# Performance work log

Measured on AMD Instinct MI355X. Metric: run time of the kernel, lower is better.

## Reference

```python
import jax, jax.numpy as jnp
import numpy as np

B, T, EMB, HS = 4, 4096, 1024, 64
BASE = 10000.0


def rope_angles(T, hs, base=BASE):
    # theta_i = base^(-2i/hs), freqs[t, i] = t * theta_i  -> (T, hs//2)
    inv = 1.0 / (base ** (2.0 * jnp.arange(hs // 2, dtype=jnp.float32) / hs))
    return jnp.arange(T, dtype=jnp.float32)[:, None] * inv[None, :]


def apply_rope(x, cos, sin):
    # x: (B, T, D); pairs are interleaved (even, odd) like torch.view_as_complex
    xr = x.reshape(*x.shape[:-1], -1, 2)
    xe, xo = xr[..., 0], xr[..., 1]
    re = xe * cos - xo * sin
    im = xe * sin + xo * cos
    return jnp.stack([re, im], axis=-1).reshape(x.shape)


def setup_inputs() -> dict:
    key = jax.random.key(0)
    kx, kq, kk, kv = jax.random.split(key, 4)
    s = 1.0 / np.sqrt(EMB)
    return {
        "x": jax.random.normal(kx, (B, T, EMB), jnp.float32),
        "Wq": jax.random.normal(kq, (HS, EMB), jnp.float32) * s,
        "Wk": jax.random.normal(kk, (HS, EMB), jnp.float32) * s,
        "Wv": jax.random.normal(kv, (HS, EMB), jnp.float32) * s,
    }


def reference(x, Wq, Wk, Wv):
    Tlen = x.shape[1]
    ang = rope_angles(Tlen, HS)          # (T, HS//2)
    cos, sin = jnp.cos(ang), jnp.sin(ang)
    q = x @ Wq.T                          # (B, T, HS)
    k = x @ Wk.T
    v = x @ Wv.T
    q = apply_rope(q, cos, sin)
    k = apply_rope(k, cos, sin)
    scores = jnp.einsum("bqd,bkd->bqk", q, k) * (HS ** -0.5)
    causal = jnp.tril(jnp.ones((Tlen, Tlen), dtype=bool))
    scores = jnp.where(causal[None], scores, -jnp.inf)
    w = jax.nn.softmax(scores, axis=-1)   # dropout in eval mode: identity
    return jnp.einsum("bqk,bkd->bqd", w, v)
```

## Files before the change

### kernel.cpp

```cpp
#include <hip/hip_runtime.h>

typedef __bf16 bf16x8 __attribute__((ext_vector_type(8)));
typedef __bf16 bf16x4 __attribute__((ext_vector_type(4)));
typedef float f32x4 __attribute__((ext_vector_type(4)));
typedef float f32x16 __attribute__((ext_vector_type(16)));
typedef unsigned int u32;

#define T_LEN 4096

__device__ __forceinline__ f32x4 mfma16(bf16x8 a, bf16x8 b, f32x4 c) {
    return __builtin_amdgcn_mfma_f32_16x16x32_bf16(a, b, c, 0, 0, 0);
}
__device__ __forceinline__ f32x16 mfma32(bf16x8 a, bf16x8 b, f32x16 c) {
    return __builtin_amdgcn_mfma_f32_32x32x16_bf16(a, b, c, 0, 0, 0);
}
__device__ __forceinline__ u32 packbf(float lo, float hi) {
    union { __bf16 e[2]; u32 w; } u;
    u.e[0] = (__bf16)lo; u.e[1] = (__bf16)hi;
    return u.w;
}
__device__ __forceinline__ f32x16 zero16() {
    f32x16 z;
    #pragma unroll
    for (int i = 0; i < 16; i++) z[i] = 0.f;
    return z;
}

__global__ __launch_bounds__(256) void convert_w_kernel(
    const float* __restrict__ Wq, const float* __restrict__ Wk,
    const float* __restrict__ Wv, __bf16* __restrict__ wf)
{
    int e = (blockIdx.x * 256 + threadIdx.x) * 4;
    int frag = e >> 9;
    int wi = e & 511;
    int l = wi >> 3, j = wi & 7;
    int ft = frag / 12, fn = frag - ft * 12;
    int n = fn * 16 + (l & 15);
    int k = (ft >> 1) * 64 + (ft & 1) * 32 + ((l >> 4) & 3) * 8 + j;
    const float* src = (n < 64 ? Wq : (n < 128 ? Wk : Wv))
                     + (size_t)(n & 63) * 1024 + k;
    float4 f = *(const float4*)src;
    bf16x4 h = {(__bf16)f.x, (__bf16)f.y, (__bf16)f.z, (__bf16)f.w};
    *(bf16x4*)(wf + e) = h;
}

__global__ __launch_bounds__(512, 2) void proj_kernel(
    const float* __restrict__ x, const __bf16* __restrict__ wf,
    __bf16* __restrict__ qfb, __bf16* __restrict__ kfb, __bf16* __restrict__ vfb)
{
    __shared__ __bf16 smem[6144];
    __bf16 (*xs)[32][72] = (__bf16(*)[32][72])smem;
    __bf16* stage = smem;

    const int tid  = threadIdx.x;
    const int wave = tid >> 6, lane = tid & 63;
    const int l15 = lane & 15, l4 = lane >> 4;
    const int wm = wave >> 2, wn = wave & 3;
    const size_t m0 = (size_t)blockIdx.x * 32;
    const int xrow = tid >> 4, xc4 = (tid & 15) * 4;

    f32x4 acc[3];
    #pragma unroll
    for (int bn = 0; bn < 3; bn++) acc[bn] = (f32x4){0.f, 0.f, 0.f, 0.f};

    const float* xsrc = x + (m0 + xrow) * 1024 + xc4;
    const __bf16* wfw = wf + (size_t)(wn * 3) * 512 + lane * 8;

    float4 rxA, rxB;
    bf16x8 wA[3][2], wB[3][2];

    {
        float4 r0 = *(const float4*)(xsrc);
        bf16x4 hx = {(__bf16)r0.x, (__bf16)r0.y, (__bf16)r0.z, (__bf16)r0.w};
        *(bf16x4*)&xs[0][xrow][xc4] = hx;
        rxA = *(const float4*)(xsrc + 64);
        #pragma unroll
        for (int nf = 0; nf < 3; nf++)
            #pragma unroll
            for (int c = 0; c < 2; c++)
                wA[nf][c] = *(const bf16x8*)(wfw + (size_t)(c * 12 + nf) * 512);
    }
    __syncthreads();

    for (int t = 0; t < 16; t++) {
        const int cur = t & 1;
        if (t < 14)
            rxB = *(const float4*)(xsrc + (t + 2) * 64);
        if (t < 15) {
            const __bf16* wnx = wfw + (size_t)((t + 1) * 2) * 12 * 512;
            #pragma unroll
            for (int nf = 0; nf < 3; nf++)
                #pragma unroll
                for (int c = 0; c < 2; c++)
                    wB[nf][c] = *(const bf16x8*)(wnx + (size_t)(c * 12 + nf) * 512);
        }
        bf16x8 af[2];
        #pragma unroll
        for (int c = 0; c < 2; c++)
            af[c] = *(const bf16x8*)&xs[cur][wm * 16 + l15][c * 32 + l4 * 8];
        #pragma unroll
        for (int nf = 0; nf < 3; nf++)
            #pragma unroll
            for (int c = 0; c < 2; c++)
                acc[nf] = mfma16(af[c], wA[nf][c], acc[nf]);
        if (t < 15) {
            bf16x4 hx = {(__bf16)rxA.x, (__bf16)rxA.y, (__bf16)rxA.z, (__bf16)rxA.w};
            *(bf16x4*)&xs[cur ^ 1][xrow][xc4] = hx;
        }
        #pragma unroll
        for (int nf = 0; nf < 3; nf++)
            #pragma unroll
            for (int c = 0; c < 2; c++)
                wA[nf][c] = wB[nf][c];
        rxA = rxB;
        __syncthreads();
    }

    const int tq0 = (int)(m0 & 4095);
    #pragma unroll
    for (int nf = 0; nf < 3; nf++) {
        int n = wn * 48 + nf * 16 + l15;
        #pragma unroll
        for (int r = 0; r < 4; r++) {
            int row = wm * 16 + l4 * 4 + r;
            float val = acc[nf][r];
            float partner = __shfl_xor(val, 1);
            if (n < 128) {
                int i = (n & 63) >> 1;
                float ang = (float)(tq0 + row)
                          * __builtin_exp2f((float)i * (-13.287712379549449f / 32.f));
                float sn, cs;
                __sincosf(ang, &sn, &cs);
                float res = (n & 1) ? (partner * sn + val * cs)
                                    : (val * cs - partner * sn);
                if (n < 64) {
                    res *= 0.180336884f;
                    int d = n;
                    stage[(d >> 4) * 512 + (row + ((d >> 3) & 1) * 32) * 8 + (d & 7)]
                        = (__bf16)res;
                } else {
                    int d = n - 64;
                    int l31i = ((row >> 2) & 1) * 16 + ((row >> 4) & 1) * 8
                             + ((row >> 3) & 1) * 4 + (row & 3);
                    stage[2048 + (d >> 4) * 512
                          + (l31i + ((d >> 3) & 1) * 32) * 8 + (d & 7)] = (__bf16)res;
                }
            } else {
                int d = n - 128;
                int cc = ((d >> 5) << 1) | ((row & 31) >> 4);
                stage[4096 + cc * 512
                      + ((d & 31) + ((row >> 3) & 1) * 32) * 8 + (row & 7)]
                    = (__bf16)val;
            }
        }
    }
    __syncthreads();
    {
        const size_t bbase = (size_t)(m0 >> 12) * 262144;
        const size_t tbase = (size_t)((m0 & 4095) >> 5) * 2048;
        bf16x4 q4 = *(const bf16x4*)&stage[tid * 4];
        bf16x4 k4 = *(const bf16x4*)&stage[2048 + tid * 4];
        bf16x4 v4 = *(const bf16x4*)&stage[4096 + tid * 4];
        *(bf16x4*)(qfb + bbase + tbase + tid * 4) = q4;
        *(bf16x4*)(kfb + bbase + tbase + tid * 4) = k4;
        *(bf16x4*)(vfb + bbase + tbase + tid * 4) = v4;
    }
}

__global__ __launch_bounds__(1024) void flash_kernel(
    const __bf16* __restrict__ qfb, const __bf16* __restrict__ kfb,
    const __bf16* __restrict__ vfb, float* __restrict__ out)
{
    __shared__ float ods[16][32][36];
    __shared__ float mls[2][16][32];

    const int tid = threadIdx.x;
    const int wave = tid >> 6, lane = tid & 63;
    const int l31 = lane & 31, h = lane >> 5;
    const int xcd = blockIdx.x & 7;
    const int b = xcd >> 1;
    const int p = ((blockIdx.x >> 3) << 1) | (xcd & 1);

    const __bf16* qb_b = qfb + (size_t)b * 262144;
    const __bf16* kb_b = kfb + (size_t)b * 262144;
    const __bf16* vb_b = vfb + (size_t)b * 262144;

    #pragma unroll 1
    for (int half = 0; half < 2; half++) {
        const int jt = half ? p : 127 - p;
        const int q0 = jt * 32;
        const int qg = q0 + l31;

        const __bf16* qp = qb_b + (size_t)jt * 2048 + lane * 8;
        bf16x8 qf[4];
        #pragma unroll
        for (int dc = 0; dc < 4; dc++) qf[dc] = *(const bf16x8*)(qp + dc * 512);

        float m = 16.f, l = 0.f;
        f32x16 o0 = zero16(), o1 = zero16();
        const int nt = jt + 1;

        #pragma unroll 1
        for (int kt = wave; kt < nt; kt += 16) {
            const int kc0 = kt << 5;
            const __bf16* kr = kb_b + (size_t)kt * 2048 + lane * 8;
            bf16x8 kf0 = *(const bf16x8*)(kr);
            bf16x8 kf1 = *(const bf16x8*)(kr + 512);
            bf16x8 kf2 = *(const bf16x8*)(kr + 1024);
            bf16x8 kf3 = *(const bf16x8*)(kr + 1536);
            const __bf16* vr = vb_b + (size_t)kt * 2048 + lane * 8;
            bf16x8 vf00 = *(const bf16x8*)(vr);
            bf16x8 vf01 = *(const bf16x8*)(vr + 512);
            bf16x8 vf10 = *(const bf16x8*)(vr + 1024);
            bf16x8 vf11 = *(const bf16x8*)(vr + 1536);
            f32x16 s = zero16();
            __builtin_amdgcn_s_setprio(1);
            s = mfma32(kf0, qf[0], s);
            s = mfma32(kf1, qf[1], s);
            s = mfma32(kf2, qf[2], s);
            s = mfma32(kf3, qf[3], s);
            __builtin_amdgcn_s_setprio(0);
            if (kt == jt) {
                #pragma unroll
                for (int r = 0; r < 16; r++) {
                    int pioff = ((r >> 2) & 1) * 16 + 8 * h + (r >> 3) * 4 + (r & 3);
                    if (kc0 + pioff > qg) s[r] = -1e30f;
                }
            }
            float tm[8];
            #pragma unroll
            for (int i = 0; i < 8; i++) tm[i] = fmaxf(s[2 * i], s[2 * i + 1]);
            #pragma unroll
            for (int i = 0; i < 4; i++) tm[i] = fmaxf(tm[i], tm[i + 4]);
            float tmax = fmaxf(fmaxf(tm[0], tm[1]), fmaxf(tm[2], tm[3]));
            float ts[4] = {0.f, 0.f, 0.f, 0.f};
            #pragma unroll
            for (int r = 0; r < 16; r++) {
                float e = __builtin_exp2f(s[r] - m);
                s[r] = e;
                ts[r & 3] += e;
            }
            float lsum = (ts[0] + ts[1]) + (ts[2] + ts[3]);
            float lsum_p = __shfl_xor(lsum, 32);
            float tmax_p = __shfl_xor(tmax, 32);
            union { u32 w[4]; bf16x8 v; } pf[2];
            #pragma unroll
            for (int cg = 0; cg < 2; cg++) {
                pf[cg].w[0] = packbf(s[4 * cg + 0],  s[4 * cg + 1]);
                pf[cg].w[1] = packbf(s[4 * cg + 2],  s[4 * cg + 3]);
                pf[cg].w[2] = packbf(s[4 * cg + 8],  s[4 * cg + 9]);
                pf[cg].w[3] = packbf(s[4 * cg + 10], s[4 * cg + 11]);
            }
            __builtin_amdgcn_s_setprio(1);
            o0 = mfma32(vf00, pf[0].v, o0);
            o0 = mfma32(vf01, pf[1].v, o0);
            o1 = mfma32(vf10, pf[0].v, o1);
            o1 = mfma32(vf11, pf[1].v, o1);
            __builtin_amdgcn_s_setprio(0);
            l += lsum + lsum_p;
            float tmx = fmaxf(tmax, tmax_p);
            if (!__all(tmx <= m + 8.f)) {
                const float mnew = fmaxf(m, tmx);
                const float alpha = __builtin_exp2f(m - mnew);
                m = mnew;
                l *= alpha;
                #pragma unroll
                for (int r = 0; r < 16; r++) { o0[r] *= alpha; o1[r] *= alpha; }
            }
        }

        const int q = tid >> 5, dcm = tid & 31;
        #pragma unroll
        for (int c2 = 0; c2 < 4; c2++) {
            f32x4 w0 = {o0[4 * c2], o0[4 * c2 + 1], o0[4 * c2 + 2], o0[4 * c2 + 3]};
            *(f32x4*)&ods[wave][l31][8 * c2 + 4 * h] = w0;
        }
        if (h == 0) {
            mls[0][wave][l31] = (wave < nt) ? m : -1e30f;
            mls[1][wave][l31] = l;
        }
        __syncthreads();
        float M = -1e30f;
        #pragma unroll
        for (int s2 = 0; s2 < 16; s2++) M = fmaxf(M, mls[0][s2][q]);
        float w16[16], L = 0.f;
        #pragma unroll
        for (int s2 = 0; s2 < 16; s2++) {
            float ws = __builtin_exp2f(mls[0][s2][q] - M);
            w16[s2] = ws;
            L += ws * mls[1][s2][q];
        }
        const float invL = 1.f / L;
        float accA = 0.f;
        #pragma unroll
        for (int s2 = 0; s2 < 16; s2++) accA += w16[s2] * ods[s2][q][dcm];
        out[((size_t)b * T_LEN + q0 + q) * 64 + dcm] = accA * invL;
        __syncthreads();
        #pragma unroll
        for (int c2 = 0; c2 < 4; c2++) {
            f32x4 w1 = {o1[4 * c2], o1[4 * c2 + 1], o1[4 * c2 + 2], o1[4 * c2 + 3]};
            *(f32x4*)&ods[wave][l31][8 * c2 + 4 * h] = w1;
        }
        __syncthreads();
        float accB = 0.f;
        #pragma unroll
        for (int s2 = 0; s2 < 16; s2++) accB += w16[s2] * ods[s2][q][dcm];
        out[((size_t)b * T_LEN + q0 + q) * 64 + 32 + dcm] = accB * invL;
        __syncthreads();
    }
}

extern "C" void kernel_launch(void* const* d_in, const int* in_sizes, int n_in,
                              void* d_out, int out_size, void* d_ws, size_t ws_size,
                              hipStream_t stream)
{
    const float* x  = (const float*)d_in[0];
    const float* Wq = (const float*)d_in[1];
    const float* Wk = (const float*)d_in[2];
    const float* Wv = (const float*)d_in[3];
    float* out = (float*)d_out;

    __bf16* qfb = (__bf16*)d_ws;
    __bf16* kfb = qfb + 1048576;
    __bf16* vfb = kfb + 1048576;
    __bf16* wf  = vfb + 1048576;

    convert_w_kernel<<<192, 256, 0, stream>>>(Wq, Wk, Wv, wf);
    proj_kernel<<<512, 512, 0, stream>>>(x, wf, qfb, kfb, vfb);
    flash_kernel<<<256, 1024, 0, stream>>>(qfb, kfb, vfb, out);
}
```

Measured before the change: 55.74 us.

## Restructure projection kernel: 16-row tiles, full x row staged in LDS

The projection kernel now uses 16-row blocks of 256 threads (1024 blocks). Each block loads its entire 16x1024 x slice into LDS as bf16 up front, then runs a straight K loop that streams weight fragments from global memory, replacing the double-buffered x/W pipeline. The weight fragment layout is reindexed to a linear 32-wide k ordering, and the output staging and stores are reworked so half-tiles of 16 rows write the correct portions of the 32-row packed Q/K/V layouts. This is meant to raise parallelism and simplify the loop. In exchange each weight fragment is read by twice as many blocks, and there is no prefetch overlap of weight loads with the MFMAs.

```diff
diff --git a/kernel.cpp b/kernel.cpp
--- a/kernel.cpp
+++ b/kernel.cpp
@@ -36,7 +36,7 @@
     int l = wi >> 3, j = wi & 7;
     int ft = frag / 12, fn = frag - ft * 12;
     int n = fn * 16 + (l & 15);
-    int k = (ft >> 1) * 64 + (ft & 1) * 32 + ((l >> 4) & 3) * 8 + j;
+    int k = ft * 32 + ((l >> 4) & 3) * 8 + j;
     const float* src = (n < 64 ? Wq : (n < 128 ? Wk : Wv))
                      + (size_t)(n & 63) * 1024 + k;
     float4 f = *(const float4*)src;
@@ -44,90 +44,62 @@
     *(bf16x4*)(wf + e) = h;
 }
 
-__global__ __launch_bounds__(512, 2) void proj_kernel(
+__global__ __launch_bounds__(256) void proj_kernel(
     const float* __restrict__ x, const __bf16* __restrict__ wf,
     __bf16* __restrict__ qfb, __bf16* __restrict__ kfb, __bf16* __restrict__ vfb)
 {
-    __shared__ __bf16 smem[6144];
-    __bf16 (*xs)[32][72] = (__bf16(*)[32][72])smem;
-    __bf16* stage = smem;
-
+    __shared__ __bf16 smem[16512];
     const int tid  = threadIdx.x;
     const int wave = tid >> 6, lane = tid & 63;
     const int l15 = lane & 15, l4 = lane >> 4;
-    const int wm = wave >> 2, wn = wave & 3;
-    const size_t m0 = (size_t)blockIdx.x * 32;
-    const int xrow = tid >> 4, xc4 = (tid & 15) * 4;
+    const size_t m0 = (size_t)blockIdx.x * 16;
+
+    {
+        const int row = tid >> 4, c0 = (tid & 15) * 64;
+        const float* src = x + (m0 + row) * 1024 + c0;
+        __bf16* dst = smem + row * 1032 + c0;
+        #pragma unroll
+        for (int u = 0; u < 8; u++) {
+            float4 f0 = *(const float4*)(src + u * 8);
+            float4 f1 = *(const float4*)(src + u * 8 + 4);
+            bf16x8 h = {(__bf16)f0.x, (__bf16)f0.y, (__bf16)f0.z, (__bf16)f0.w,
+                        (__bf16)f1.x, (__bf16)f1.y, (__bf16)f1.z, (__bf16)f1.w};
+            *(bf16x8*)(dst + u * 8) = h;
+        }
+    }
+    __syncthreads();
 
     f32x4 acc[3];
     #pragma unroll
-    for (int bn = 0; bn < 3; bn++) acc[bn] = (f32x4){0.f, 0.f, 0.f, 0.f};
-
-    const float* xsrc = x + (m0 + xrow) * 1024 + xc4;
-    const __bf16* wfw = wf + (size_t)(wn * 3) * 512 + lane * 8;
-
-    float4 rxA, rxB;
-    bf16x8 wA[3][2], wB[3][2];
-
-    {
-        float4 r0 = *(const float4*)(xsrc);
-        bf16x4 hx = {(__bf16)r0.x, (__bf16)r0.y, (__bf16)r0.z, (__bf16)r0.w};
-        *(bf16x4*)&xs[0][xrow][xc4] = hx;
-        rxA = *(const float4*)(xsrc + 64);
-        #pragma unroll
-        for (int nf = 0; nf < 3; nf++)
-            #pragma unroll
-            for (int c = 0; c < 2; c++)
-                wA[nf][c] = *(const bf16x8*)(wfw + (size_t)(c * 12 + nf) * 512);
+    for (int nf = 0; nf < 3; nf++) acc[nf] = (f32x4){0.f, 0.f, 0.f, 0.f};
+    const __bf16* wfw = wf + (size_t)(wave * 3) * 512 + lane * 8;
+    const __bf16* xls = smem + l15 * 1032 + l4 * 8;
+    #pragma unroll 4
+    for (int ks = 0; ks < 32; ks++) {
+        bf16x8 af = *(const bf16x8*)(xls + ks * 32);
+        const __bf16* wp = wfw + (size_t)(ks * 12) * 512;
+        #pragma unroll
+        for (int nf = 0; nf < 3; nf++) {
+            bf16x8 bw = *(const bf16x8*)(wp + (size_t)nf * 512);
+            acc[nf] = mfma16(af, bw, acc[nf]);
+        }
     }
     __syncthreads();
 
-    for (int t = 0; t < 16; t++) {
-        const int cur = t & 1;
-        if (t < 14)
-            rxB = *(const float4*)(xsrc + (t + 2) * 64);
-        if (t < 15) {
-            const __bf16* wnx = wfw + (size_t)((t + 1) * 2) * 12 * 512;
-            #pragma unroll
-            for (int nf = 0; nf < 3; nf++)
-                #pragma unroll
-                for (int c = 0; c < 2; c++)
-                    wB[nf][c] = *(const bf16x8*)(wnx + (size_t)(c * 12 + nf) * 512);
-        }
-        bf16x8 af[2];
-        #pragma unroll
-        for (int c = 0; c < 2; c++)
-            af[c] = *(const bf16x8*)&xs[cur][wm * 16 + l15][c * 32 + l4 * 8];
-        #pragma unroll
-        for (int nf = 0; nf < 3; nf++)
-            #pragma unroll
-            for (int c = 0; c < 2; c++)
-                acc[nf] = mfma16(af[c], wA[nf][c], acc[nf]);
-        if (t < 15) {
-            bf16x4 hx = {(__bf16)rxA.x, (__bf16)rxA.y, (__bf16)rxA.z, (__bf16)rxA.w};
-            *(bf16x4*)&xs[cur ^ 1][xrow][xc4] = hx;
-        }
-        #pragma unroll
-        for (int nf = 0; nf < 3; nf++)
-            #pragma unroll
-            for (int c = 0; c < 2; c++)
-                wA[nf][c] = wB[nf][c];
-        rxA = rxB;
-        __syncthreads();
-    }
-
     const int tq0 = (int)(m0 & 4095);
+    const int h16 = (int)((m0 >> 4) & 1);
     #pragma unroll
     for (int nf = 0; nf < 3; nf++) {
-        int n = wn * 48 + nf * 16 + l15;
+        int n = wave * 48 + nf * 16 + l15;
         #pragma unroll
         for (int r = 0; r < 4; r++) {
-            int row = wm * 16 + l4 * 4 + r;
+            int row16 = l4 * 4 + r;
+            int row32 = h16 * 16 + row16;
             float val = acc[nf][r];
             float partner = __shfl_xor(val, 1);
             if (n < 128) {
                 int i = (n & 63) >> 1;
-                float ang = (float)(tq0 + row)
+                float ang = (float)(tq0 + row16)
                           * __builtin_exp2f((float)i * (-13.287712379549449f / 32.f));
                 float sn, cs;
                 __sincosf(ang, &sn, &cs);
@@ -136,34 +108,45 @@
                 if (n < 64) {
                     res *= 0.180336884f;
                     int d = n;
-                    stage[(d >> 4) * 512 + (row + ((d >> 3) & 1) * 32) * 8 + (d & 7)]
+                    smem[(d >> 4) * 512 + (row32 + ((d >> 3) & 1) * 32) * 8 + (d & 7)]
                         = (__bf16)res;
                 } else {
                     int d = n - 64;
-                    int l31i = ((row >> 2) & 1) * 16 + ((row >> 4) & 1) * 8
-                             + ((row >> 3) & 1) * 4 + (row & 3);
-                    stage[2048 + (d >> 4) * 512
-                          + (l31i + ((d >> 3) & 1) * 32) * 8 + (d & 7)] = (__bf16)res;
+                    int l31i = ((row32 >> 2) & 1) * 16 + ((row32 >> 4) & 1) * 8
+                             + ((row32 >> 3) & 1) * 4 + (row32 & 3);
+                    smem[2048 + (d >> 4) * 512
+                         + (l31i + ((d >> 3) & 1) * 32) * 8 + (d & 7)] = (__bf16)res;
                 }
             } else {
                 int d = n - 128;
-                int cc = ((d >> 5) << 1) | ((row & 31) >> 4);
-                stage[4096 + cc * 512
-                      + ((d & 31) + ((row >> 3) & 1) * 32) * 8 + (row & 7)]
+                int cc = ((d >> 5) << 1) | ((row32 & 31) >> 4);
+                smem[4096 + cc * 512
+                     + ((d & 31) + ((row32 >> 3) & 1) * 32) * 8 + (row32 & 7)]
                     = (__bf16)val;
             }
         }
     }
     __syncthreads();
+
     {
         const size_t bbase = (size_t)(m0 >> 12) * 262144;
         const size_t tbase = (size_t)((m0 & 4095) >> 5) * 2048;
-        bf16x4 q4 = *(const bf16x4*)&stage[tid * 4];
-        bf16x4 k4 = *(const bf16x4*)&stage[2048 + tid * 4];
-        bf16x4 v4 = *(const bf16x4*)&stage[4096 + tid * 4];
-        *(bf16x4*)(qfb + bbase + tbase + tid * 4) = q4;
-        *(bf16x4*)(kfb + bbase + tbase + tid * 4) = k4;
-        *(bf16x4*)(vfb + bbase + tbase + tid * 4) = v4;
+        {
+            int rq = tid >> 5;
+            int off = (rq >> 1) * 512 + (rq & 1) * 256 + h16 * 128 + (tid & 31) * 4;
+            *(bf16x4*)(qfb + bbase + tbase + off) = *(const bf16x4*)&smem[off];
+        }
+        {
+            int rk = tid >> 4;
+            int off = (rk >> 2) * 512 + ((rk >> 1) & 1) * 256 + (rk & 1) * 128
+                    + h16 * 64 + (tid & 15) * 4;
+            *(bf16x4*)(kfb + bbase + tbase + off) = *(const bf16x4*)&smem[2048 + off];
+        }
+        {
+            int part = tid >> 7;
+            int off = part * 1024 + h16 * 512 + (tid & 127) * 4;
+            *(bf16x4*)(vfb + bbase + tbase + off) = *(const bf16x4*)&smem[4096 + off];
+        }
     }
 }
 
@@ -326,6 +309,6 @@
     __bf16* wf  = vfb + 1048576;
 
     convert_w_kernel<<<192, 256, 0, stream>>>(Wq, Wk, Wv, wf);
-    proj_kernel<<<512, 512, 0, stream>>>(x, wf, qfb, kfb, vfb);
+    proj_kernel<<<1024, 256, 0, stream>>>(x, wf, qfb, kfb, vfb);
     flash_kernel<<<256, 1024, 0, stream>>>(qfb, kfb, vfb, out);
 }
```

After: 59.58 us. 1.07x slower.
